# Kernel optimization log

Hardware: AMD Instinct MI355X
Metric: run time of the kernel (lower is better)

The kernel has to match this reference:

```python
import jax, jax.numpy as jnp
import numpy as np

B = 4
N1_PER = 16384  # fine points per scene
N2_PER = 4096   # coarse points per scene
IN_PLANES = 512
OUT_PLANES = 256
K = 3
CHUNK = 2048
BN_EPS = 1e-5


def _bn(x, g, b, m, v):
    # eval-mode BatchNorm1d: affine normalize with running stats
    return (x - m) * (g / jnp.sqrt(v + BN_EPS)) + b


def _interpolate_one(p1b, p2b, f2b):
    # p1b: [n1,3] queries, p2b: [n2,3] support, f2b: [n2,C]
    # k=3 inverse-distance weighted interpolation (pointops.interpolation)
    pq = p1b.reshape(-1, CHUNK, 3)  # chunk queries to avoid full [n1,n2] matrix

    def step(carry, q):  # q: [CHUNK,3]
        d2 = jnp.sum((q[:, None, :] - p2b[None, :, :]) ** 2, axis=-1)  # [CHUNK,n2]
        neg_d2, idx = jax.lax.top_k(-d2, K)                            # [CHUNK,K]
        dist = jnp.sqrt(jnp.maximum(-neg_d2, 1e-12))
        w = 1.0 / (dist + 1e-8)
        w = w / jnp.sum(w, axis=-1, keepdims=True)
        feat = f2b[idx]  # [CHUNK,K,C] gather
        return carry, jnp.einsum('qk,qkc->qc', w, feat)

    _, out = jax.lax.scan(step, None, pq)
    return out.reshape(-1, f2b.shape[-1])  # [n1,C]


def _forward(p1, x1, p2, x2, W1, b1, g1, be1, m1, v1, W2, b2, g2, be2, m2, v2):
    # branch 1: Linear-BN-ReLU on fine features
    h1 = jax.nn.relu(_bn(x1 @ W1.T + b1, g1, be1, m1, v1))  # [N1, out]
    # branch 2: Linear-BN-ReLU on coarse features, then kNN interpolation up
    h2 = jax.nn.relu(_bn(x2 @ W2.T + b2, g2, be2, m2, v2))  # [N2, out]
    # equal-sized scenes -> reshape + vmap over batch (offsets are [n,2n,...])
    p1b = p1.reshape(B, N1_PER, 3)
    p2b = p2.reshape(B, N2_PER, 3)
    h2b = h2.reshape(B, N2_PER, -1)
    up = jax.vmap(_interpolate_one)(p1b, p2b, h2b).reshape(-1, h2.shape[-1])
    return h1 + up


def setup_inputs() -> dict:
    key = jax.random.key(0)
    ks = jax.random.split(key, 16)
    p1 = jax.random.normal(ks[0], (B * N1_PER, 3), dtype=jnp.float32)
    x1 = jax.random.normal(ks[1], (B * N1_PER, OUT_PLANES), dtype=jnp.float32)
    p2 = jax.random.normal(ks[2], (B * N2_PER, 3), dtype=jnp.float32)
    x2 = jax.random.normal(ks[3], (B * N2_PER, IN_PLANES), dtype=jnp.float32)
    o1 = (jnp.arange(1, B + 1) * N1_PER).astype(jnp.int64)
    o2 = (jnp.arange(1, B + 1) * N2_PER).astype(jnp.int64)
    s1 = 1.0 / np.sqrt(OUT_PLANES)
    s2 = 1.0 / np.sqrt(IN_PLANES)
    W1 = jax.random.uniform(ks[4], (OUT_PLANES, OUT_PLANES), minval=-s1, maxval=s1)
    b1 = jax.random.uniform(ks[5], (OUT_PLANES,), minval=-s1, maxval=s1)
    W2 = jax.random.uniform(ks[6], (OUT_PLANES, IN_PLANES), minval=-s2, maxval=s2)
    b2 = jax.random.uniform(ks[7], (OUT_PLANES,), minval=-s2, maxval=s2)
    g1 = jnp.ones((OUT_PLANES,)); be1 = jnp.zeros((OUT_PLANES,))
    m1 = 0.1 * jax.random.normal(ks[8], (OUT_PLANES,))
    v1 = jax.random.uniform(ks[9], (OUT_PLANES,), minval=0.5, maxval=1.5)
    g2 = jnp.ones((OUT_PLANES,)); be2 = jnp.zeros((OUT_PLANES,))
    m2 = 0.1 * jax.random.normal(ks[10], (OUT_PLANES,))
    v2 = jax.random.uniform(ks[11], (OUT_PLANES,), minval=0.5, maxval=1.5)
    return dict(p1=p1, x1=x1, p2=p2, x2=x2, W1=W1, b1=b1, g1=g1, be1=be1,
                m1=m1, v1=v1, W2=W2, b2=b2, g2=g2, be2=be2, m2=m2, v2=v2,
                o1=o1, o2=o2)


def reference(p1, x1, p2, x2, W1, b1, g1, be1, m1, v1, W2, b2, g2, be2, m2, v2, o1, o2):
    return _forward(p1, x1, p2, x2, W1, b1, g1, be1, m1, v1, W2, b2, g2, be2, m2, v2)
```

## Files before the change

### kernel.cpp

```cpp
#include <hip/hip_runtime.h>

#define BM 128
#define BNT 128
#define BK 32
#define LDK 40

typedef __bf16 bf16x8 __attribute__((ext_vector_type(8)));
typedef float  f32x4  __attribute__((ext_vector_type(4)));
typedef float  f32x2  __attribute__((ext_vector_type(2)));

static __device__ __forceinline__ unsigned short f2bf(float f) {
  union { float f; unsigned int i; } c; c.f = f;
  unsigned int u = c.i;
  u += 0x7FFFu + ((u >> 16) & 1u);
  return (unsigned short)(u >> 16);
}

#define SEG0 16777216u
#define SEG1 25165824u
#define SEG2 25231360u
#define SEG3 25362432u

__global__ __launch_bounds__(256) void cvt4_k(const float* __restrict__ s0,
                                              const float* __restrict__ s1,
                                              const float* __restrict__ s2,
                                              const float* __restrict__ s3,
                                              unsigned short* __restrict__ dst) {
  const unsigned int e = (blockIdx.x * 256u + threadIdx.x) * 8u;
  const float* sp; unsigned int off;
  if (e < SEG0)      { sp = s0; off = e; }
  else if (e < SEG1) { sp = s1; off = e - SEG0; }
  else if (e < SEG2) { sp = s2; off = e - SEG1; }
  else               { sp = s3; off = e - SEG2; }
  const float4* p = (const float4*)(sp + off);
  const float4 a = p[0], b = p[1];
  uint4 o;
  o.x = ((unsigned int)f2bf(a.y) << 16) | f2bf(a.x);
  o.y = ((unsigned int)f2bf(a.w) << 16) | f2bf(a.z);
  o.z = ((unsigned int)f2bf(b.y) << 16) | f2bf(b.x);
  o.w = ((unsigned int)f2bf(b.w) << 16) | f2bf(b.z);
  *(uint4*)(dst + e) = o;
}

template<bool FUSE>
__global__ __launch_bounds__(256) void gemm_bn_relu_k(
    const unsigned short* __restrict__ A,
    const unsigned short* __restrict__ Wm,
    const float* __restrict__ bias,
    const float* __restrict__ gam,
    const float* __restrict__ bet,
    const float* __restrict__ rmean,
    const float* __restrict__ rvar,
    const int K,
    float* __restrict__ outp,
    const float* __restrict__ h2f,
    const float* __restrict__ wgt,
    const int* __restrict__ idxg)
{
  __shared__ unsigned short As[BM][LDK];
  __shared__ unsigned short Bs[BNT][LDK];
  __shared__ float SC[BNT];
  __shared__ float SH[BNT];
  __shared__ float Wt[BM * 3];
  __shared__ int   Id[BM * 3];

  const int tid = threadIdx.x;
  const int bm = blockIdx.x, bn = blockIdx.y;

  if (tid < BNT) {
    const int ch = bn * BNT + tid;
    const float sc = gam[ch] / sqrtf(rvar[ch] + 1e-5f);
    SC[tid] = sc;
    SH[tid] = (bias[ch] - rmean[ch]) * sc + bet[ch];
  }
  if (FUSE) {
    for (int i = tid; i < BM * 3; i += 256) {
      Wt[i] = wgt[bm * (BM * 3) + i];
      Id[i] = idxg[bm * (BM * 3) + i];
    }
  }

  const int wave = tid >> 6, lane = tid & 63;
  const int wr = (wave >> 1) * 64, wc = (wave & 1) * 64;
  const int lr = lane & 15;
  const int kq = (lane >> 4) * 8;

  const int r0 = tid >> 2, co = (tid & 3) * 8;
  const int r1 = 64 + r0;
  const unsigned short* Ar0 = A + (size_t)(bm * BM + r0) * K + co;
  const unsigned short* Ar1 = A + (size_t)(bm * BM + r1) * K + co;
  const unsigned short* Br0 = Wm + (size_t)(bn * BNT + r0) * K + co;
  const unsigned short* Br1 = Wm + (size_t)(bn * BNT + r1) * K + co;

  f32x4 acc[4][4];
  const f32x4 zero = {0.f, 0.f, 0.f, 0.f};
#pragma unroll
  for (int i = 0; i < 4; ++i)
#pragma unroll
    for (int j = 0; j < 4; ++j) acc[i][j] = zero;

  uint4 va0 = *(const uint4*)(Ar0);
  uint4 va1 = *(const uint4*)(Ar1);
  uint4 vb0 = *(const uint4*)(Br0);
  uint4 vb1 = *(const uint4*)(Br1);

  for (int k0 = 0; k0 < K; k0 += BK) {
    __syncthreads();
    *(uint4*)&As[r0][co] = va0;
    *(uint4*)&As[r1][co] = va1;
    *(uint4*)&Bs[r0][co] = vb0;
    *(uint4*)&Bs[r1][co] = vb1;
    __syncthreads();
    if (k0 + BK < K) {
      va0 = *(const uint4*)(Ar0 + k0 + BK);
      va1 = *(const uint4*)(Ar1 + k0 + BK);
      vb0 = *(const uint4*)(Br0 + k0 + BK);
      vb1 = *(const uint4*)(Br1 + k0 + BK);
    }
    bf16x8 af[4], bv[4];
#pragma unroll
    for (int mi = 0; mi < 4; ++mi)
      af[mi] = *(const bf16x8*)&As[wr + mi * 16 + lr][kq];
#pragma unroll
    for (int ni = 0; ni < 4; ++ni)
      bv[ni] = *(const bf16x8*)&Bs[wc + ni * 16 + lr][kq];
#pragma unroll
    for (int mi = 0; mi < 4; ++mi)
#pragma unroll
      for (int ni = 0; ni < 4; ++ni)
        acc[mi][ni] = __builtin_amdgcn_mfma_f32_16x16x32_bf16(af[mi], bv[ni], acc[mi][ni], 0, 0, 0);
  }

#pragma unroll
  for (int mi = 0; mi < 4; ++mi) {
#pragma unroll
    for (int r = 0; r < 4; ++r) {
      const int rloc = wr + mi * 16 + (lane >> 4) * 4 + r;
      const size_t grow = (size_t)(bm * BM + rloc);
      float w0 = 0.f, w1 = 0.f, w2 = 0.f;
      const float *g0 = nullptr, *g1 = nullptr, *g2 = nullptr;
      if (FUSE) {
        w0 = Wt[rloc * 3 + 0]; w1 = Wt[rloc * 3 + 1]; w2 = Wt[rloc * 3 + 2];
        g0 = h2f + (size_t)Id[rloc * 3 + 0] * 256;
        g1 = h2f + (size_t)Id[rloc * 3 + 1] * 256;
        g2 = h2f + (size_t)Id[rloc * 3 + 2] * 256;
      }
#pragma unroll
      for (int ni = 0; ni < 4; ++ni) {
        const int cloc = wc + ni * 16 + lr;
        const int gcol = bn * BNT + cloc;
        float v = acc[mi][ni][r] * SC[cloc] + SH[cloc];
        v = fmaxf(v, 0.f);
        if (FUSE) v += w0 * g0[gcol] + w1 * g1[gcol] + w2 * g2[gcol];
        outp[grow * 256 + gcol] = v;
      }
    }
  }
}

__global__ __launch_bounds__(256) void prep_pairs(const float* __restrict__ p2,
                                                  float* __restrict__ pp) {
  const int m = blockIdx.x * 256 + threadIdx.x;
  const float* s = p2 + m * 6;
  float* d = pp + m * 8;
  d[0] = s[0]; d[1] = s[3];
  d[2] = s[1]; d[3] = s[4];
  d[4] = s[2]; d[5] = s[5];
  d[6] = 0.f;  d[7] = 0.f;
}

__global__ __launch_bounds__(256) void knn_partial(const float* __restrict__ p1,
                                                   const float* __restrict__ ppair,
                                                   float* __restrict__ s_part,
                                                   int* __restrict__ i_part) {
#pragma clang fp contract(off)
  const int tid = threadIdx.x;
  const int qb = blockIdx.x, sp = blockIdx.y;
  const int scene = qb >> 6;
  const int pbase = scene * 4096 + sp * 512;
  const int qi = qb * 256 + tid;

  const float qx = p1[qi * 3 + 0];
  const float qy = p1[qi * 3 + 1];
  const float qz = p1[qi * 3 + 2];
  const f32x2 qxx = {qx, qx}, qyy = {qy, qy}, qzz = {qz, qz};

  float s0 = 1e30f, s1 = 1e30f, s2 = 1e30f;
  int i0 = pbase, i1 = pbase, i2 = pbase;

  const f32x2* pp = (const f32x2*)(ppair + (size_t)(pbase >> 1) * 8);
#pragma unroll 4
  for (int m = 0; m < 256; ++m) {
    const f32x2 X = pp[m * 4 + 0];
    const f32x2 Y = pp[m * 4 + 1];
    const f32x2 Z = pp[m * 4 + 2];
    const f32x2 dx = qxx - X;
    const f32x2 dy = qyy - Y;
    const f32x2 dz = qzz - Z;
    const f32x2 sv = (dx * dx + dy * dy) + dz * dz;
    const int jg = pbase + 2 * m;
    const float sa = sv.x, sb = sv.y;
    if (sa < s2) {
      if (sa < s1) {
        s2 = s1; i2 = i1;
        if (sa < s0) { s1 = s0; i1 = i0; s0 = sa; i0 = jg; }
        else         { s1 = sa; i1 = jg; }
      } else { s2 = sa; i2 = jg; }
    }
    if (sb < s2) {
      if (sb < s1) {
        s2 = s1; i2 = i1;
        if (sb < s0) { s1 = s0; i1 = i0; s0 = sb; i0 = jg + 1; }
        else         { s1 = sb; i1 = jg + 1; }
      } else { s2 = sb; i2 = jg + 1; }
    }
  }
  const int ob = (qi * 8 + sp) * 3;
  s_part[ob + 0] = s0; s_part[ob + 1] = s1; s_part[ob + 2] = s2;
  i_part[ob + 0] = i0; i_part[ob + 1] = i1; i_part[ob + 2] = i2;
}

__global__ __launch_bounds__(256) void knn_merge(const float* __restrict__ s_part,
                                                 const int* __restrict__ i_part,
                                                 float* __restrict__ wgt,
                                                 int* __restrict__ idxg) {
  const int qi = blockIdx.x * 256 + threadIdx.x;

  float s0 = 1e30f, s1 = 1e30f, s2 = 1e30f;
  int i0 = 0, i1 = 0, i2 = 0;
  const int base = qi * 24;
#pragma unroll
  for (int t = 0; t < 24; ++t) {
    const float s = s_part[base + t];
    const int id = i_part[base + t];
    if (s < s2) {
      if (s < s1) {
        s2 = s1; i2 = i1;
        if (s < s0) { s1 = s0; i1 = i0; s0 = s; i0 = id; }
        else        { s1 = s;  i1 = id; }
      } else { s2 = s; i2 = id; }
    }
  }
  const float d0 = sqrtf(fmaxf(s0, 1e-12f));
  const float d1 = sqrtf(fmaxf(s1, 1e-12f));
  const float d2 = sqrtf(fmaxf(s2, 1e-12f));
  float w0 = 1.f / (d0 + 1e-8f);
  float w1 = 1.f / (d1 + 1e-8f);
  float w2 = 1.f / (d2 + 1e-8f);
  const float inv = 1.f / (w0 + w1 + w2);
  wgt[qi * 3 + 0] = w0 * inv; wgt[qi * 3 + 1] = w1 * inv; wgt[qi * 3 + 2] = w2 * inv;
  idxg[qi * 3 + 0] = i0; idxg[qi * 3 + 1] = i1; idxg[qi * 3 + 2] = i2;
}

extern "C" void kernel_launch(void* const* d_in, const int* in_sizes, int n_in,
                              void* d_out, int out_size, void* d_ws, size_t ws_size,
                              hipStream_t stream) {
  const float* p1 = (const float*)d_in[0];
  const float* x1 = (const float*)d_in[1];
  const float* p2 = (const float*)d_in[2];
  const float* x2 = (const float*)d_in[3];
  const float* W1 = (const float*)d_in[4];
  const float* b1 = (const float*)d_in[5];
  const float* g1 = (const float*)d_in[6];
  const float* be1 = (const float*)d_in[7];
  const float* m1 = (const float*)d_in[8];
  const float* v1 = (const float*)d_in[9];
  const float* W2 = (const float*)d_in[10];
  const float* b2 = (const float*)d_in[11];
  const float* g2 = (const float*)d_in[12];
  const float* be2 = (const float*)d_in[13];
  const float* m2 = (const float*)d_in[14];
  const float* v2 = (const float*)d_in[15];

  char* ws = (char*)d_ws;
  unsigned short* bfb = (unsigned short*)ws;
  unsigned short* x1b = bfb;
  unsigned short* x2b = bfb + SEG0;
  unsigned short* W1b = bfb + SEG1;
  unsigned short* W2b = bfb + SEG2;
  float* s_part = (float*)(ws + 33554432);
  int*   i_part = (int*)(ws + 39845888);
  float* h2f    = (float*)(ws + 50724864);
  float* ppair  = (float*)(ws + 67502080);
  float* wgt    = (float*)(ws + 67764224);
  int*   idxg   = (int*)(ws + 68550656);

  float* outp = (float*)d_out;

  cvt4_k<<<12384, 256, 0, stream>>>(x1, x2, W1, W2, bfb);

  gemm_bn_relu_k<false><<<dim3(128, 2), 256, 0, stream>>>(
      x2b, W2b, b2, g2, be2, m2, v2, 512, h2f, nullptr, nullptr, nullptr);

  prep_pairs<<<32, 256, 0, stream>>>(p2, ppair);

  knn_partial<<<dim3(256, 8), 256, 0, stream>>>(p1, ppair, s_part, i_part);

  knn_merge<<<256, 256, 0, stream>>>(s_part, i_part, wgt, idxg);

  gemm_bn_relu_k<true><<<dim3(512, 2), 256, 0, stream>>>(
      x1b, W1b, b1, g1, be1, m1, v1, 256, outp, h2f, wgt, idxg);
}
```

Measured before the change: 337.6 us.

## Fuse fp32-to-bf16 conversion into GEMM loads and branchless kNN top-3

```diff
diff --git a/kernel.cpp b/kernel.cpp
--- a/kernel.cpp
+++ b/kernel.cpp
@@ -9,43 +9,19 @@
 typedef float  f32x4  __attribute__((ext_vector_type(4)));
 typedef float  f32x2  __attribute__((ext_vector_type(2)));
 
-static __device__ __forceinline__ unsigned short f2bf(float f) {
-  union { float f; unsigned int i; } c; c.f = f;
-  unsigned int u = c.i;
-  u += 0x7FFFu + ((u >> 16) & 1u);
-  return (unsigned short)(u >> 16);
-}
-
-#define SEG0 16777216u
-#define SEG1 25165824u
-#define SEG2 25231360u
-#define SEG3 25362432u
-
-__global__ __launch_bounds__(256) void cvt4_k(const float* __restrict__ s0,
-                                              const float* __restrict__ s1,
-                                              const float* __restrict__ s2,
-                                              const float* __restrict__ s3,
-                                              unsigned short* __restrict__ dst) {
-  const unsigned int e = (blockIdx.x * 256u + threadIdx.x) * 8u;
-  const float* sp; unsigned int off;
-  if (e < SEG0)      { sp = s0; off = e; }
-  else if (e < SEG1) { sp = s1; off = e - SEG0; }
-  else if (e < SEG2) { sp = s2; off = e - SEG1; }
-  else               { sp = s3; off = e - SEG2; }
-  const float4* p = (const float4*)(sp + off);
-  const float4 a = p[0], b = p[1];
-  uint4 o;
-  o.x = ((unsigned int)f2bf(a.y) << 16) | f2bf(a.x);
-  o.y = ((unsigned int)f2bf(a.w) << 16) | f2bf(a.z);
-  o.z = ((unsigned int)f2bf(b.y) << 16) | f2bf(b.x);
-  o.w = ((unsigned int)f2bf(b.w) << 16) | f2bf(b.z);
-  *(uint4*)(dst + e) = o;
+static __device__ __forceinline__ unsigned int pk2(float x, float y) {
+  union { __bf16 h[2]; unsigned int u; } c;
+  c.h[0] = (__bf16)x; c.h[1] = (__bf16)y;
+  return c.u;
+}
+static __device__ __forceinline__ uint4 pack8(const float4 a, const float4 b) {
+  return make_uint4(pk2(a.x, a.y), pk2(a.z, a.w), pk2(b.x, b.y), pk2(b.z, b.w));
 }
 
 template<bool FUSE>
 __global__ __launch_bounds__(256) void gemm_bn_relu_k(
-    const unsigned short* __restrict__ A,
-    const unsigned short* __restrict__ Wm,
+    const float* __restrict__ A,
+    const float* __restrict__ Wm,
     const float* __restrict__ bias,
     const float* __restrict__ gam,
     const float* __restrict__ bet,
@@ -87,10 +63,10 @@
 
   const int r0 = tid >> 2, co = (tid & 3) * 8;
   const int r1 = 64 + r0;
-  const unsigned short* Ar0 = A + (size_t)(bm * BM + r0) * K + co;
-  const unsigned short* Ar1 = A + (size_t)(bm * BM + r1) * K + co;
-  const unsigned short* Br0 = Wm + (size_t)(bn * BNT + r0) * K + co;
-  const unsigned short* Br1 = Wm + (size_t)(bn * BNT + r1) * K + co;
+  const float* Ar0 = A + (size_t)(bm * BM + r0) * K + co;
+  const float* Ar1 = A + (size_t)(bm * BM + r1) * K + co;
+  const float* Br0 = Wm + (size_t)(bn * BNT + r0) * K + co;
+  const float* Br1 = Wm + (size_t)(bn * BNT + r1) * K + co;
 
   f32x4 acc[4][4];
   const f32x4 zero = {0.f, 0.f, 0.f, 0.f};
@@ -99,23 +75,23 @@
 #pragma unroll
     for (int j = 0; j < 4; ++j) acc[i][j] = zero;
 
-  uint4 va0 = *(const uint4*)(Ar0);
-  uint4 va1 = *(const uint4*)(Ar1);
-  uint4 vb0 = *(const uint4*)(Br0);
-  uint4 vb1 = *(const uint4*)(Br1);
+  float4 a0a = *(const float4*)(Ar0),     a0b = *(const float4*)(Ar0 + 4);
+  float4 a1a = *(const float4*)(Ar1),     a1b = *(const float4*)(Ar1 + 4);
+  float4 b0a = *(const float4*)(Br0),     b0b = *(const float4*)(Br0 + 4);
+  float4 b1a = *(const float4*)(Br1),     b1b = *(const float4*)(Br1 + 4);
 
   for (int k0 = 0; k0 < K; k0 += BK) {
     __syncthreads();
-    *(uint4*)&As[r0][co] = va0;
-    *(uint4*)&As[r1][co] = va1;
-    *(uint4*)&Bs[r0][co] = vb0;
-    *(uint4*)&Bs[r1][co] = vb1;
+    *(uint4*)&As[r0][co] = pack8(a0a, a0b);
+    *(uint4*)&As[r1][co] = pack8(a1a, a1b);
+    *(uint4*)&Bs[r0][co] = pack8(b0a, b0b);
+    *(uint4*)&Bs[r1][co] = pack8(b1a, b1b);
     __syncthreads();
     if (k0 + BK < K) {
-      va0 = *(const uint4*)(Ar0 + k0 + BK);
-      va1 = *(const uint4*)(Ar1 + k0 + BK);
-      vb0 = *(const uint4*)(Br0 + k0 + BK);
-      vb1 = *(const uint4*)(Br1 + k0 + BK);
+      a0a = *(const float4*)(Ar0 + k0 + BK); a0b = *(const float4*)(Ar0 + k0 + BK + 4);
+      a1a = *(const float4*)(Ar1 + k0 + BK); a1b = *(const float4*)(Ar1 + k0 + BK + 4);
+      b0a = *(const float4*)(Br0 + k0 + BK); b0b = *(const float4*)(Br0 + k0 + BK + 4);
+      b1a = *(const float4*)(Br1 + k0 + BK); b1b = *(const float4*)(Br1 + k0 + BK + 4);
     }
     bf16x8 af[4], bv[4];
 #pragma unroll
@@ -199,20 +175,25 @@
     const f32x2 dz = qzz - Z;
     const f32x2 sv = (dx * dx + dy * dy) + dz * dz;
     const int jg = pbase + 2 * m;
-    const float sa = sv.x, sb = sv.y;
-    if (sa < s2) {
-      if (sa < s1) {
-        s2 = s1; i2 = i1;
-        if (sa < s0) { s1 = s0; i1 = i0; s0 = sa; i0 = jg; }
-        else         { s1 = sa; i1 = jg; }
-      } else { s2 = sa; i2 = jg; }
-    }
-    if (sb < s2) {
-      if (sb < s1) {
-        s2 = s1; i2 = i1;
-        if (sb < s0) { s1 = s0; i1 = i0; s0 = sb; i0 = jg + 1; }
-        else         { s1 = sb; i1 = jg + 1; }
-      } else { s2 = sb; i2 = jg + 1; }
+    {
+      const float s = sv.x; const int j = jg;
+      const bool c0 = s < s0, c1 = s < s1, c2 = s < s2;
+      const float ns2 = c1 ? s1 : (c2 ? s : s2);
+      const int   ni2 = c1 ? i1 : (c2 ? j : i2);
+      const float ns1 = c0 ? s0 : (c1 ? s : s1);
+      const int   ni1 = c0 ? i0 : (c1 ? j : i1);
+      s0 = c0 ? s : s0;  i0 = c0 ? j : i0;
+      s1 = ns1; i1 = ni1; s2 = ns2; i2 = ni2;
+    }
+    {
+      const float s = sv.y; const int j = jg + 1;
+      const bool c0 = s < s0, c1 = s < s1, c2 = s < s2;
+      const float ns2 = c1 ? s1 : (c2 ? s : s2);
+      const int   ni2 = c1 ? i1 : (c2 ? j : i2);
+      const float ns1 = c0 ? s0 : (c1 ? s : s1);
+      const int   ni1 = c0 ? i0 : (c1 ? j : i1);
+      s0 = c0 ? s : s0;  i0 = c0 ? j : i0;
+      s1 = ns1; i1 = ni1; s2 = ns2; i2 = ni2;
     }
   }
   const int ob = (qi * 8 + sp) * 3;
@@ -273,31 +254,24 @@
   const float* v2 = (const float*)d_in[15];
 
   char* ws = (char*)d_ws;
-  unsigned short* bfb = (unsigned short*)ws;
-  unsigned short* x1b = bfb;
-  unsigned short* x2b = bfb + SEG0;
-  unsigned short* W1b = bfb + SEG1;
-  unsigned short* W2b = bfb + SEG2;
-  float* s_part = (float*)(ws + 33554432);
-  int*   i_part = (int*)(ws + 39845888);
-  float* h2f    = (float*)(ws + 50724864);
-  float* ppair  = (float*)(ws + 67502080);
-  float* wgt    = (float*)(ws + 67764224);
-  int*   idxg   = (int*)(ws + 68550656);
+  float* h2f    = (float*)(ws);
+  float* ppair  = (float*)(ws + 16777216);
+  float* s_part = (float*)(ws + 17039360);
+  int*   i_part = (int*)(ws + 23330816);
+  float* wgt    = (float*)(ws + 29622272);
+  int*   idxg   = (int*)(ws + 30408704);
 
   float* outp = (float*)d_out;
 
-  cvt4_k<<<12384, 256, 0, stream>>>(x1, x2, W1, W2, bfb);
+  prep_pairs<<<32, 256, 0, stream>>>(p2, ppair);
+
+  knn_partial<<<dim3(256, 8), 256, 0, stream>>>(p1, ppair, s_part, i_part);
+
+  knn_merge<<<256, 256, 0, stream>>>(s_part, i_part, wgt, idxg);
 
   gemm_bn_relu_k<false><<<dim3(128, 2), 256, 0, stream>>>(
-      x2b, W2b, b2, g2, be2, m2, v2, 512, h2f, nullptr, nullptr, nullptr);
-
-  prep_pairs<<<32, 256, 0, stream>>>(p2, ppair);
-
-  knn_partial<<<dim3(256, 8), 256, 0, stream>>>(p1, ppair, s_part, i_part);
-
-  knn_merge<<<256, 256, 0, stream>>>(s_part, i_part, wgt, idxg);
+      x2, W2, b2, g2, be2, m2, v2, 512, h2f, nullptr, nullptr, nullptr);
 
   gemm_bn_relu_k<true><<<dim3(512, 2), 256, 0, stream>>>(
-      x1b, W1b, b1, g1, be1, m1, v1, 256, outp, h2f, wgt, idxg);
-}
+      x1, W1, b1, g1, be1, m1, v1, 256, outp, h2f, wgt, idxg);
+}
```

New measurement: 370.7 us. 9.8% more time.
